# Kernel tuning notes

Hardware: AMD Instinct MI355X
Metric: run time of the kernel (lower is better)

The kernel has to match this reference:

```python
import jax, jax.numpy as jnp
import numpy as np

NUM_TNETS = 8388608
NUM_PINS = 20971520
NUM_NODES = 1048576

def setup_inputs() -> dict:
    key = jax.random.key(0)
    k1, k2, k3 = jax.random.split(key, 3)
    beta = jax.random.uniform(k1, (1,), dtype=jnp.float32)
    tnet_weights = jax.random.uniform(k2, (NUM_TNETS,), dtype=jnp.float32)
    flat_tnet2pin = jax.random.randint(k3, (2 * NUM_TNETS,), 0, NUM_PINS, dtype=jnp.int64)
    pin2node_map = jax.random.randint(jax.random.fold_in(key, 7), (NUM_PINS,), 0, NUM_NODES, dtype=jnp.int64)
    return {
        "beta": beta,
        "tnet_weights": tnet_weights,
        "flat_tnet2pin": flat_tnet2pin,
        "pin2node_map": pin2node_map,
    }

def reference(beta, tnet_weights, flat_tnet2pin, pin2node_map):
    # flat_tnet2pin layout: [src_0, dst_0, src_1, dst_1, ...] (2 pins per timing arc)
    # gather node id for every arc pin: [2*num_tnets]
    node_idx = pin2node_map[flat_tnet2pin]
    # each arc's weight is added at both its source and sink node
    w = jnp.repeat(tnet_weights, 2)  # [w0, w0, w1, w1, ...] matches flat layout
    out = jnp.zeros(NUM_NODES, dtype=jnp.float32).at[node_idx].add(w)
    return out * beta
```

## Files before the change

kernel.cpp:

```cpp
#include <hip/hip_runtime.h>
#include <stdint.h>


#define TILE 4096
#define THREADS 512
#define IPT  8
#define NB1  40
#define SHIFT1 19
#define CAP1R 55296
#define TPB1R 14
#define NB2  64
#define SHIFT2 14
#define CAP2R 34816
#define ACC_NODES 16384
#define PARTS 8
#define CLINE_INTS 16
#define TICK1_OFF 65536
#define TICK2_OFF 66048
#define CTRL_BYTES 66560
#define NT2R (5 * 8 * TPB1R)

typedef unsigned long long item_t;
typedef int   int4_ev   __attribute__((ext_vector_type(4)));
typedef float float4_ev __attribute__((ext_vector_type(4)));
typedef unsigned long long ull2_ev __attribute__((ext_vector_type(2)));

#define BAR() do { __builtin_amdgcn_sched_barrier(0); \
    asm volatile("s_waitcnt lgkmcnt(0)" ::: "memory"); \
    __builtin_amdgcn_s_barrier(); \
    __builtin_amdgcn_sched_barrier(0); } while (0)

__device__ __forceinline__ item_t pack_item(uint32_t key, float w) {
    return (item_t)key | ((item_t)__float_as_uint(w) << 32);
}

__device__ __forceinline__ void ms_passA(item_t (&e)[IPT], int vcnt, int shift,
                                         int* hist, uint32_t (&rankp)[IPT / 2]) {
#pragma unroll
    for (int k = 0; k < IPT; ++k) {
        int b = (int)((uint32_t)e[k] >> shift);
        uint32_t rr = (k < vcnt) ? (uint32_t)atomicAdd(&hist[b], 1) : 0u;
        if ((k & 1) == 0) rankp[k >> 1] = rr;
        else              rankp[k >> 1] |= (rr << 16);
    }
}

__device__ __forceinline__ void ms_scan(int t, int* hist, unsigned long long* combo,
                                        int* wsum, int* gcur, int gcur_stride) {
    int val = (t < 256) ? hist[t] : 0;
    int inc = val;
#pragma unroll
    for (int d = 1; d < 64; d <<= 1) {
        int n = __shfl_up(inc, d, 64);
        if ((t & 63) >= d) inc += n;
    }
    if (t < 256 && (t & 63) == 63) wsum[t >> 6] = inc;
    BAR();
    if (t < 256) {
        hist[t] = 0;
        int w = t >> 6, prefix = 0;
        if (w > 0) prefix += wsum[0];
        if (w > 1) prefix += wsum[1];
        if (w > 2) prefix += wsum[2];
        int bx = prefix + inc - val;
        int gb = (val > 0) ? atomicAdd(&gcur[t * gcur_stride], val) : 0;
        combo[t] = ((unsigned long long)(uint32_t)gb << 32) | (uint32_t)bx;
    }
}

__device__ __forceinline__ void ms_passD(item_t (&e)[IPT], int vcnt, int shift,
                                         uint32_t (&rankp)[IPT / 2],
                                         unsigned long long* combo, item_t* stage) {
#pragma unroll
    for (int k = 0; k < IPT; ++k) {
        if (k < vcnt) {
            int b = (int)((uint32_t)e[k] >> shift);
            int rr = (int)((rankp[k >> 1] >> ((k & 1) * 16)) & 0xffffu);
            stage[(int)((uint32_t)combo[b]) + rr] = e[k];
        }
    }
}

__device__ __forceinline__ void ms_passE(int t, item_t* stage, int tile_cnt, int shift,
                                         unsigned long long* combo,
                                         item_t* gout, size_t bin_stride, size_t cap) {
    for (int j = t; j < tile_cnt; j += THREADS) {
        item_t ev = stage[j];
        int b = (int)((uint32_t)(ev & 0xffffffffull) >> shift);
        unsigned long long c = combo[b];
        long long dst = (long long)(int)(c >> 32) + (j - (int)(uint32_t)c);
        if (dst >= 0 && dst < (long long)cap)
            __builtin_nontemporal_store(ev, &gout[(size_t)b * bin_stride + (size_t)dst]);
    }
}

__global__ __launch_bounds__(THREADS, 8) void k1_partition_pins(
    const int* __restrict__ flat_pins, const float* __restrict__ weights,
    int* __restrict__ ctrl1, int* __restrict__ tick1,
    item_t* __restrict__ items1, int total)
{
    __shared__ int hist[256];
    __shared__ unsigned long long combo[256];
    __shared__ int wsum[4];
    __shared__ item_t stage[TILE];
    __shared__ int sh_tk;

    const int t = threadIdx.x;
    const int r = blockIdx.x & 7;
    const int gridTiles = (total + TILE - 1) / TILE;
    const int ntr = (gridTiles > r) ? ((gridTiles - r + 7) >> 3) : 0;
    int* mytick = tick1 + r * CLINE_INTS;
    int* mycur  = ctrl1 + r * CLINE_INTS;
    item_t* mout = items1 + (size_t)r * CAP1R;

    if (t == 0) sh_tk = atomicAdd(mytick, 1);
    if (t < 256) hist[t] = 0;
    __syncthreads();
    if (sh_tk >= ntr) return;

    item_t e[IPT];
    int vcnt, tcnt;
    {
        int tb = (r + (sh_tk << 3)) * TILE;
        int base = tb + t * IPT;
        tcnt = min(TILE, total - tb);
        if (base + IPT <= total) {
            vcnt = IPT;
            int4_ev p0 = __builtin_nontemporal_load((const int4_ev*)(flat_pins + base));
            int4_ev p1 = __builtin_nontemporal_load((const int4_ev*)(flat_pins + base) + 1);
            float4_ev w = __builtin_nontemporal_load((const float4_ev*)(weights + (base >> 1)));
#pragma unroll
            for (int k = 0; k < IPT; ++k)
                e[k] = pack_item((uint32_t)((k < 4) ? p0[k & 3] : p1[k & 3]), w[(k >> 1) & 3]);
        } else {
            int rem = total - base;
            vcnt = rem < 0 ? 0 : (rem > IPT ? IPT : rem);
#pragma unroll
            for (int k = 0; k < IPT; ++k) {
                int i = base + k;
                e[k] = (i < total) ? pack_item((uint32_t)flat_pins[i], weights[i >> 1]) : 0ull;
            }
        }
    }
    __syncthreads();

    for (;;) {
        int tkf = 0x7fffffff;
        if (t == 0) tkf = atomicAdd(mytick, 1);
        uint32_t rankp[IPT / 2];
        ms_passA(e, vcnt, SHIFT1, hist, rankp);
        BAR();
        ms_scan(t, hist, combo, wsum, mycur, 8 * CLINE_INTS);
        if (t == 0) sh_tk = tkf;
        BAR();
        ms_passD(e, vcnt, SHIFT1, rankp, combo, stage);
        BAR();
        const int tkn = sh_tk;
        const bool valid = (tkn < ntr);
        int4_ev px0, px1; float4_ev wx;
        bool fastN = false; int baseN = 0, tbN = 0;
        if (valid) {
            tbN = (r + (tkn << 3)) * TILE;
            baseN = tbN + t * IPT;
            fastN = (baseN + IPT <= total);
            if (fastN) {
                px0 = __builtin_nontemporal_load((const int4_ev*)(flat_pins + baseN));
                px1 = __builtin_nontemporal_load((const int4_ev*)(flat_pins + baseN) + 1);
                wx  = __builtin_nontemporal_load((const float4_ev*)(weights + (baseN >> 1)));
            }
        }
        ms_passE(t, stage, tcnt, SHIFT1, combo, mout, (size_t)8 * CAP1R, (size_t)CAP1R);
        BAR();
        if (!valid) break;
        tcnt = min(TILE, total - tbN);
        if (fastN) {
            vcnt = IPT;
#pragma unroll
            for (int k = 0; k < IPT; ++k)
                e[k] = pack_item((uint32_t)((k < 4) ? px0[k & 3] : px1[k & 3]), wx[(k >> 1) & 3]);
        } else {
            int rem = total - baseN;
            vcnt = rem < 0 ? 0 : (rem > IPT ? IPT : rem);
#pragma unroll
            for (int k = 0; k < IPT; ++k) {
                int i = baseN + k;
                e[k] = (i < total) ? pack_item((uint32_t)flat_pins[i], weights[i >> 1]) : 0ull;
            }
        }
    }
}

__global__ __launch_bounds__(THREADS, 8) void k2_gather_partition(
    const item_t* __restrict__ items1, const int* __restrict__ ctrl1,
    const int* __restrict__ pin2node, int* __restrict__ ctrl2,
    int* __restrict__ tick2, item_t* __restrict__ items2)
{
    __shared__ int hist[256];
    __shared__ unsigned long long combo[256];
    __shared__ int wsum[4];
    __shared__ item_t stage[TILE];
    __shared__ int sh_tk;
    __shared__ int sh_cnt[NB1];

    const int t = threadIdx.x;
    const int r2 = blockIdx.x & 7;
    int* mytick = tick2 + r2 * CLINE_INTS;
    int* mycur  = ctrl2 + r2 * CLINE_INTS;
    item_t* mout = items2 + (size_t)r2 * CAP2R;

    if (t == 0) sh_tk = atomicAdd(mytick, 1);
    if (t < 256) hist[t] = 0;
    if (t < NB1) {
        int bin = r2 + 8 * (t >> 3);
        sh_cnt[t] = min(ctrl1[(bin * 8 + (t & 7)) * CLINE_INTS], (int)CAP1R);
    }
    __syncthreads();
    if (sh_tk >= NT2R) return;

#define GMERGE(slot, ev_) { item_t ev = (ev_); \
        int nd = pin2node[(uint32_t)ev]; \
        e[slot] = (ev & 0xffffffff00000000ull) | (uint32_t)nd; }

    item_t e[IPT];
    int vcnt, tcnt;
    {
        int tk = sh_tk;
        int g = tk / (8 * TPB1R), rem = tk % (8 * TPB1R);
        int r_w = rem / TPB1R, tile = rem % TPB1R;
        int bin = r2 + 8 * g;
        int cnt = sh_cnt[(g << 3) | r_w];
        int tb = tile * TILE;
        tcnt = max(0, min(TILE, cnt - tb));
        const item_t* src = items1 + ((size_t)bin * 8 + (size_t)r_w) * CAP1R;
        int base = tb + t * IPT;
        if (base + IPT <= cnt) {
            vcnt = IPT;
            ull2_ev x0 = __builtin_nontemporal_load((const ull2_ev*)(src + base));
            ull2_ev x1 = __builtin_nontemporal_load((const ull2_ev*)(src + base) + 1);
            ull2_ev x2 = __builtin_nontemporal_load((const ull2_ev*)(src + base) + 2);
            ull2_ev x3 = __builtin_nontemporal_load((const ull2_ev*)(src + base) + 3);
            GMERGE(0, x0[0]) GMERGE(1, x0[1]) GMERGE(2, x1[0]) GMERGE(3, x1[1])
            GMERGE(4, x2[0]) GMERGE(5, x2[1]) GMERGE(6, x3[0]) GMERGE(7, x3[1])
        } else {
            int rem2 = cnt - base;
            vcnt = rem2 < 0 ? 0 : (rem2 > IPT ? IPT : rem2);
#pragma unroll
            for (int k = 0; k < IPT; ++k) {
                int i = base + k;
                if (i >= 0 && i < cnt) { GMERGE(k, src[i]) } else e[k] = 0ull;
            }
        }
    }
    __syncthreads();

    for (;;) {
        int tkf = 0x7fffffff;
        if (t == 0) tkf = atomicAdd(mytick, 1);
        uint32_t rankp[IPT / 2];
        ms_passA(e, vcnt, SHIFT2, hist, rankp);
        BAR();
        ms_scan(t, hist, combo, wsum, mycur, 8 * CLINE_INTS);
        if (t == 0) sh_tk = tkf;
        BAR();
        ms_passD(e, vcnt, SHIFT2, rankp, combo, stage);
        BAR();
        const int tkn = sh_tk;
        const bool valid = (tkn < NT2R);
        ull2_ev nx0, nx1, nx2, nx3;
        bool fastN = false;
        const item_t* srcN = items1;
        int baseN = 0, cntN = 0, tbN = 0;
        if (valid) {
            int g = tkn / (8 * TPB1R), rem = tkn % (8 * TPB1R);
            int r_w = rem / TPB1R, tile = rem % TPB1R;
            int bin = r2 + 8 * g;
            cntN = sh_cnt[(g << 3) | r_w];
            tbN = tile * TILE;
            srcN = items1 + ((size_t)bin * 8 + (size_t)r_w) * CAP1R;
            baseN = tbN + t * IPT;
            fastN = (baseN + IPT <= cntN);
            if (fastN) {
                nx0 = __builtin_nontemporal_load((const ull2_ev*)(srcN + baseN));
                nx1 = __builtin_nontemporal_load((const ull2_ev*)(srcN + baseN) + 1);
                nx2 = __builtin_nontemporal_load((const ull2_ev*)(srcN + baseN) + 2);
                nx3 = __builtin_nontemporal_load((const ull2_ev*)(srcN + baseN) + 3);
            }
        }
        ms_passE(t, stage, tcnt, SHIFT2, combo, mout, (size_t)8 * CAP2R, (size_t)CAP2R);
        BAR();
        if (!valid) break;
        tcnt = max(0, min(TILE, cntN - tbN));
        if (fastN) {
            vcnt = IPT;
            GMERGE(0, nx0[0]) GMERGE(1, nx0[1]) GMERGE(2, nx1[0]) GMERGE(3, nx1[1])
            GMERGE(4, nx2[0]) GMERGE(5, nx2[1]) GMERGE(6, nx3[0]) GMERGE(7, nx3[1])
        } else {
            int rem2 = cntN - baseN;
            vcnt = rem2 < 0 ? 0 : (rem2 > IPT ? IPT : rem2);
#pragma unroll
            for (int k = 0; k < IPT; ++k) {
                int i = baseN + k;
                if (i >= 0 && i < cntN) { GMERGE(k, srcN[i]) } else e[k] = 0ull;
            }
        }
    }
#undef GMERGE
}

__global__ __launch_bounds__(1024, 8) void k3_accumulate_part(
    const item_t* __restrict__ items2, const int* __restrict__ ctrl2,
    float* __restrict__ partials)
{
    __shared__ float acc[ACC_NODES];
    const int b = blockIdx.x >> 3;
    const int p = blockIdx.x & (PARTS - 1);
    const int t = threadIdx.x;
    for (int i = t; i < ACC_NODES; i += 1024) acc[i] = 0.f;
    __syncthreads();

    const int cnt = min(ctrl2[(b * 8 + p) * CLINE_INTS], (int)CAP2R);
    const item_t* src = items2 + ((size_t)b * 8 + (size_t)p) * CAP2R;
    const ull2_ev* src2 = (const ull2_ev*)src;
    const int npair = cnt >> 1;
    const int quarter = npair >> 2;

#define K3_LOAD(A0, A1, A2, A3, g) { \
    A0 = __builtin_nontemporal_load(src2 + (g)); \
    A1 = __builtin_nontemporal_load(src2 + quarter + (g)); \
    A2 = __builtin_nontemporal_load(src2 + 2 * quarter + (g)); \
    A3 = __builtin_nontemporal_load(src2 + 3 * quarter + (g)); }
#define K3_ACC1(ev) atomicAdd(&acc[(uint32_t)(ev) & (ACC_NODES - 1)], \
                              __uint_as_float((uint32_t)((ev) >> 32)))
#define K3_PROC(A0, A1, A2, A3) { \
    K3_ACC1(A0[0]); K3_ACC1(A0[1]); K3_ACC1(A1[0]); K3_ACC1(A1[1]); \
    K3_ACC1(A2[0]); K3_ACC1(A2[1]); K3_ACC1(A3[0]); K3_ACC1(A3[1]); }

    ull2_ev a0, a1, a2, a3, b0, b1, b2, b3;
    int g = t;
    bool vA = g < quarter;
    if (vA) K3_LOAD(a0, a1, a2, a3, g)
    int gB = g + 1024;
    while (vA) {
        bool vB = gB < quarter;
        if (vB) K3_LOAD(b0, b1, b2, b3, gB)
        K3_PROC(a0, a1, a2, a3)
        g = gB + 1024;
        vA = g < quarter;
        if (vA) K3_LOAD(a0, a1, a2, a3, g)
        if (vB) K3_PROC(b0, b1, b2, b3)
        gB = g + 1024;
    }
    for (int i = (quarter << 3) + t; i < cnt; i += 1024) {
        item_t ev = src[i];
        K3_ACC1(ev);
    }
#undef K3_LOAD
#undef K3_ACC1
#undef K3_PROC
    __syncthreads();
    float* __restrict__ dst = partials + (size_t)blockIdx.x * ACC_NODES;
    for (int i = t; i < ACC_NODES; i += 1024) dst[i] = acc[i];
}

__global__ __launch_bounds__(256) void k4_reduce(
    const float* __restrict__ partials, const float* __restrict__ beta,
    float* __restrict__ out, int num_nodes)
{
    const float bt = beta[0];
    const int n = (blockIdx.x * 256 + threadIdx.x) << 2;
    if (n + 3 < num_nodes) {
        const int b   = n >> SHIFT2;
        const int off = n & (ACC_NODES - 1);
        const float* base = partials + ((size_t)b * PARTS) * ACC_NODES + off;
        float4_ev s = {0.f, 0.f, 0.f, 0.f};
#pragma unroll
        for (int p = 0; p < PARTS; ++p)
            s += *(const float4_ev*)(base + (size_t)p * ACC_NODES);
        *(float4_ev*)(out + n) = s * bt;
    } else {
        for (int k = 0; k < 4; ++k) {
            int nn = n + k;
            if (nn < num_nodes) {
                const int b   = nn >> SHIFT2;
                const int off = nn & (ACC_NODES - 1);
                float s = 0.f;
#pragma unroll
                for (int p = 0; p < PARTS; ++p)
                    s += partials[((size_t)b * PARTS + p) * ACC_NODES + off];
                out[nn] = s * bt;
            }
        }
    }
}

__global__ __launch_bounds__(256) void scatter_device(
    const float* __restrict__ beta, const float* __restrict__ tnet_weights,
    const long long* __restrict__ pin_pairs, const int* __restrict__ pin2node_map,
    float* __restrict__ out, int num_tnets)
{
    int t = blockIdx.x * blockDim.x + threadIdx.x;
    if (t >= num_tnets) return;
    long long pp = pin_pairs[t];
    float w = tnet_weights[t] * beta[0];
    atomicAdd(&out[pin2node_map[(int)(pp & 0xffffffffLL)]], w);
    atomicAdd(&out[pin2node_map[(int)(pp >> 32)]], w);
}

extern "C" void kernel_launch(void* const* d_in, const int* in_sizes, int n_in,
                              void* d_out, int out_size, void* d_ws, size_t ws_size,
                              hipStream_t stream) {
    const float* beta         = (const float*)d_in[0];
    const float* weights      = (const float*)d_in[1];
    const int*   flat_pins    = (const int*)d_in[2];
    const int*   pin2node     = (const int*)d_in[3];
    float* out = (float*)d_out;

    const int num_tnets = in_sizes[1];
    const int total     = in_sizes[2];
    const int num_nodes = out_size;

    const size_t items1Bytes = (size_t)NB1 * 8 * CAP1R * sizeof(item_t);
    const size_t items2Bytes = (size_t)NB2 * 8 * CAP2R * sizeof(item_t);
    const size_t partBytes   = (size_t)NB2 * PARTS * ACC_NODES * sizeof(float);

    int* ctrl1 = (int*)d_ws;
    int* ctrl2 = (int*)((char*)d_ws + 32768);
    int* tick1 = (int*)((char*)d_ws + TICK1_OFF);
    int* tick2 = (int*)((char*)d_ws + TICK2_OFF);

    if (ws_size >= CTRL_BYTES + items1Bytes + items2Bytes + partBytes) {
        item_t* items1 = (item_t*)((char*)d_ws + CTRL_BYTES);
        item_t* items2 = (item_t*)((char*)d_ws + CTRL_BYTES + items1Bytes);
        float*  partials = (float*)((char*)d_ws + CTRL_BYTES + items1Bytes + items2Bytes);
        (void)hipMemsetAsync(d_ws, 0, CTRL_BYTES, stream);
        k1_partition_pins<<<1024, THREADS, 0, stream>>>(
            flat_pins, weights, ctrl1, tick1, items1, total);
        k2_gather_partition<<<1024, THREADS, 0, stream>>>(
            items1, ctrl1, pin2node, ctrl2, tick2, items2);
        k3_accumulate_part<<<NB2 * PARTS, 1024, 0, stream>>>(
            items2, ctrl2, partials);
        const int i4slots = (num_nodes + 3) / 4;
        k4_reduce<<<(i4slots + 255) / 256, 256, 0, stream>>>(
            partials, beta, out, num_nodes);
    } else {
        (void)hipMemsetAsync(d_out, 0, (size_t)out_size * sizeof(float), stream);
        scatter_device<<<(num_tnets + 255) / 256, 256, 0, stream>>>(
            beta, weights, (const long long*)flat_pins, pin2node, out, num_tnets);
    }
}
```

Before: 464.6 us.

## Replace atomic ticket work-stealing with static two-tile-per-block assignment in partition kernels

The persistent 1024-block grids in the first two partition kernels, which grab tiles through per-residue atomic tickets, are replaced by grids sized so each block handles exactly two statically assigned tiles. The next tile's loads are still issued before the scatter of the current tile. This removes the per-iteration atomic ticket traffic and the tick counters in the workspace, which also shrinks the memset. In exchange it launches many more blocks, pays per-block setup and histogram init again for each pair of tiles, and loses dynamic load balancing.

After: 466.5 us. No clear change (+0.4%).

```diff
diff --git a/kernel.cpp b/kernel.cpp
--- a/kernel.cpp
+++ b/kernel.cpp
@@ -15,10 +15,8 @@
 #define ACC_NODES 16384
 #define PARTS 8
 #define CLINE_INTS 16
-#define TICK1_OFF 65536
-#define TICK2_OFF 66048
-#define CTRL_BYTES 66560
-#define NT2R (5 * 8 * TPB1R)
+#define CTRL_BYTES 65536
+#define SPR2 (5 * 8 * TPB1R)
 
 typedef unsigned long long item_t;
 typedef int   int4_ev   __attribute__((ext_vector_type(4)));
@@ -94,216 +92,153 @@
     }
 }
 
+__device__ __forceinline__ void k1_load(
+    const int* __restrict__ flat_pins, const float* __restrict__ weights,
+    int total, int tb, int t, item_t (&e)[IPT], int& vcnt, int& tcnt)
+{
+    const int base = tb + t * IPT;
+    int tc = total - tb; tc = tc < 0 ? 0 : (tc > TILE ? TILE : tc);
+    tcnt = tc;
+    if (base + IPT <= total) {
+        vcnt = IPT;
+        int4_ev p0 = __builtin_nontemporal_load((const int4_ev*)(flat_pins + base));
+        int4_ev p1 = __builtin_nontemporal_load((const int4_ev*)(flat_pins + base) + 1);
+        float4_ev w = __builtin_nontemporal_load((const float4_ev*)(weights + (base >> 1)));
+#pragma unroll
+        for (int k = 0; k < IPT; ++k)
+            e[k] = pack_item((uint32_t)((k < 4) ? p0[k & 3] : p1[k & 3]), w[(k >> 1) & 3]);
+    } else {
+        int rem = total - base;
+        vcnt = rem < 0 ? 0 : (rem > IPT ? IPT : rem);
+#pragma unroll
+        for (int k = 0; k < IPT; ++k) {
+            int i = base + k;
+            e[k] = (i < total) ? pack_item((uint32_t)flat_pins[i], weights[i >> 1]) : 0ull;
+        }
+    }
+}
+
 __global__ __launch_bounds__(THREADS, 8) void k1_partition_pins(
     const int* __restrict__ flat_pins, const float* __restrict__ weights,
-    int* __restrict__ ctrl1, int* __restrict__ tick1,
-    item_t* __restrict__ items1, int total)
+    int* __restrict__ ctrl1, item_t* __restrict__ items1, int total)
 {
     __shared__ int hist[256];
     __shared__ unsigned long long combo[256];
     __shared__ int wsum[4];
     __shared__ item_t stage[TILE];
-    __shared__ int sh_tk;
 
     const int t = threadIdx.x;
     const int r = blockIdx.x & 7;
-    const int gridTiles = (total + TILE - 1) / TILE;
-    const int ntr = (gridTiles > r) ? ((gridTiles - r + 7) >> 3) : 0;
-    int* mytick = tick1 + r * CLINE_INTS;
-    int* mycur  = ctrl1 + r * CLINE_INTS;
+    const int sp = blockIdx.x >> 3;
+    int* mycur = ctrl1 + r * CLINE_INTS;
     item_t* mout = items1 + (size_t)r * CAP1R;
 
-    if (t == 0) sh_tk = atomicAdd(mytick, 1);
     if (t < 256) hist[t] = 0;
-    __syncthreads();
-    if (sh_tk >= ntr) return;
 
     item_t e[IPT];
     int vcnt, tcnt;
-    {
-        int tb = (r + (sh_tk << 3)) * TILE;
-        int base = tb + t * IPT;
-        tcnt = min(TILE, total - tb);
-        if (base + IPT <= total) {
-            vcnt = IPT;
-            int4_ev p0 = __builtin_nontemporal_load((const int4_ev*)(flat_pins + base));
-            int4_ev p1 = __builtin_nontemporal_load((const int4_ev*)(flat_pins + base) + 1);
-            float4_ev w = __builtin_nontemporal_load((const float4_ev*)(weights + (base >> 1)));
-#pragma unroll
-            for (int k = 0; k < IPT; ++k)
-                e[k] = pack_item((uint32_t)((k < 4) ? p0[k & 3] : p1[k & 3]), w[(k >> 1) & 3]);
-        } else {
-            int rem = total - base;
-            vcnt = rem < 0 ? 0 : (rem > IPT ? IPT : rem);
-#pragma unroll
-            for (int k = 0; k < IPT; ++k) {
-                int i = base + k;
-                e[k] = (i < total) ? pack_item((uint32_t)flat_pins[i], weights[i >> 1]) : 0ull;
-            }
-        }
-    }
+    const int j0 = r + 8 * (2 * sp);
+    k1_load(flat_pins, weights, total, j0 * TILE, t, e, vcnt, tcnt);
     __syncthreads();
 
-    for (;;) {
-        int tkf = 0x7fffffff;
-        if (t == 0) tkf = atomicAdd(mytick, 1);
+#pragma unroll 1
+    for (int it = 0; it < 2; ++it) {
         uint32_t rankp[IPT / 2];
         ms_passA(e, vcnt, SHIFT1, hist, rankp);
         BAR();
         ms_scan(t, hist, combo, wsum, mycur, 8 * CLINE_INTS);
-        if (t == 0) sh_tk = tkf;
         BAR();
         ms_passD(e, vcnt, SHIFT1, rankp, combo, stage);
         BAR();
-        const int tkn = sh_tk;
-        const bool valid = (tkn < ntr);
-        int4_ev px0, px1; float4_ev wx;
-        bool fastN = false; int baseN = 0, tbN = 0;
-        if (valid) {
-            tbN = (r + (tkn << 3)) * TILE;
-            baseN = tbN + t * IPT;
-            fastN = (baseN + IPT <= total);
-            if (fastN) {
-                px0 = __builtin_nontemporal_load((const int4_ev*)(flat_pins + baseN));
-                px1 = __builtin_nontemporal_load((const int4_ev*)(flat_pins + baseN) + 1);
-                wx  = __builtin_nontemporal_load((const float4_ev*)(weights + (baseN >> 1)));
-            }
-        }
-        ms_passE(t, stage, tcnt, SHIFT1, combo, mout, (size_t)8 * CAP1R, (size_t)CAP1R);
-        BAR();
-        if (!valid) break;
-        tcnt = min(TILE, total - tbN);
-        if (fastN) {
-            vcnt = IPT;
-#pragma unroll
-            for (int k = 0; k < IPT; ++k)
-                e[k] = pack_item((uint32_t)((k < 4) ? px0[k & 3] : px1[k & 3]), wx[(k >> 1) & 3]);
-        } else {
-            int rem = total - baseN;
-            vcnt = rem < 0 ? 0 : (rem > IPT ? IPT : rem);
-#pragma unroll
-            for (int k = 0; k < IPT; ++k) {
-                int i = baseN + k;
-                e[k] = (i < total) ? pack_item((uint32_t)flat_pins[i], weights[i >> 1]) : 0ull;
-            }
-        }
+        const int tcnt_cur = tcnt;
+        if (it == 0) {
+            k1_load(flat_pins, weights, total, (j0 + 8) * TILE, t, e, vcnt, tcnt);
+        }
+        ms_passE(t, stage, tcnt_cur, SHIFT1, combo, mout,
+                 (size_t)8 * CAP1R, (size_t)CAP1R);
+        BAR();
     }
 }
 
 __global__ __launch_bounds__(THREADS, 8) void k2_gather_partition(
     const item_t* __restrict__ items1, const int* __restrict__ ctrl1,
-    const int* __restrict__ pin2node, int* __restrict__ ctrl2,
-    int* __restrict__ tick2, item_t* __restrict__ items2)
+    const int* __restrict__ pin2node,
+    int* __restrict__ ctrl2, item_t* __restrict__ items2)
 {
     __shared__ int hist[256];
     __shared__ unsigned long long combo[256];
     __shared__ int wsum[4];
     __shared__ item_t stage[TILE];
-    __shared__ int sh_tk;
     __shared__ int sh_cnt[NB1];
 
     const int t = threadIdx.x;
     const int r2 = blockIdx.x & 7;
-    int* mytick = tick2 + r2 * CLINE_INTS;
-    int* mycur  = ctrl2 + r2 * CLINE_INTS;
+    const int sp = blockIdx.x >> 3;
+    int* mycur = ctrl2 + r2 * CLINE_INTS;
     item_t* mout = items2 + (size_t)r2 * CAP2R;
 
-    if (t == 0) sh_tk = atomicAdd(mytick, 1);
     if (t < 256) hist[t] = 0;
     if (t < NB1) {
         int bin = r2 + 8 * (t >> 3);
         sh_cnt[t] = min(ctrl1[(bin * 8 + (t & 7)) * CLINE_INTS], (int)CAP1R);
     }
     __syncthreads();
-    if (sh_tk >= NT2R) return;
 
 #define GMERGE(slot, ev_) { item_t ev = (ev_); \
         int nd = pin2node[(uint32_t)ev]; \
         e[slot] = (ev & 0xffffffff00000000ull) | (uint32_t)nd; }
 
+#define K2_LOAD(sidx) { \
+        int s_ = (sidx); \
+        int g_ = s_ / (8 * TPB1R), rem_ = s_ % (8 * TPB1R); \
+        int rw_ = rem_ / TPB1R, tile_ = rem_ % TPB1R; \
+        int bin_ = r2 + 8 * g_; \
+        int cnt_ = sh_cnt[(g_ << 3) | rw_]; \
+        int tb_ = tile_ * TILE; \
+        int tc_ = cnt_ - tb_; tc_ = tc_ < 0 ? 0 : (tc_ > TILE ? TILE : tc_); \
+        tcnt = tc_; \
+        const item_t* src_ = items1 + ((size_t)bin_ * 8 + (size_t)rw_) * CAP1R; \
+        int base_ = tb_ + t * IPT; \
+        if (base_ + IPT <= cnt_) { \
+            vcnt = IPT; \
+            ull2_ev x0 = __builtin_nontemporal_load((const ull2_ev*)(src_ + base_)); \
+            ull2_ev x1 = __builtin_nontemporal_load((const ull2_ev*)(src_ + base_) + 1); \
+            ull2_ev x2 = __builtin_nontemporal_load((const ull2_ev*)(src_ + base_) + 2); \
+            ull2_ev x3 = __builtin_nontemporal_load((const ull2_ev*)(src_ + base_) + 3); \
+            GMERGE(0, x0[0]) GMERGE(1, x0[1]) GMERGE(2, x1[0]) GMERGE(3, x1[1]) \
+            GMERGE(4, x2[0]) GMERGE(5, x2[1]) GMERGE(6, x3[0]) GMERGE(7, x3[1]) \
+        } else { \
+            int rem2_ = cnt_ - base_; \
+            vcnt = rem2_ < 0 ? 0 : (rem2_ > IPT ? IPT : rem2_); \
+            _Pragma("unroll") \
+            for (int k = 0; k < IPT; ++k) { \
+                int i_ = base_ + k; \
+                if (i_ < cnt_) { GMERGE(k, src_[i_]) } else e[k] = 0ull; \
+            } \
+        } }
+
     item_t e[IPT];
     int vcnt, tcnt;
-    {
-        int tk = sh_tk;
-        int g = tk / (8 * TPB1R), rem = tk % (8 * TPB1R);
-        int r_w = rem / TPB1R, tile = rem % TPB1R;
-        int bin = r2 + 8 * g;
-        int cnt = sh_cnt[(g << 3) | r_w];
-        int tb = tile * TILE;
-        tcnt = max(0, min(TILE, cnt - tb));
-        const item_t* src = items1 + ((size_t)bin * 8 + (size_t)r_w) * CAP1R;
-        int base = tb + t * IPT;
-        if (base + IPT <= cnt) {
-            vcnt = IPT;
-            ull2_ev x0 = __builtin_nontemporal_load((const ull2_ev*)(src + base));
-            ull2_ev x1 = __builtin_nontemporal_load((const ull2_ev*)(src + base) + 1);
-            ull2_ev x2 = __builtin_nontemporal_load((const ull2_ev*)(src + base) + 2);
-            ull2_ev x3 = __builtin_nontemporal_load((const ull2_ev*)(src + base) + 3);
-            GMERGE(0, x0[0]) GMERGE(1, x0[1]) GMERGE(2, x1[0]) GMERGE(3, x1[1])
-            GMERGE(4, x2[0]) GMERGE(5, x2[1]) GMERGE(6, x3[0]) GMERGE(7, x3[1])
-        } else {
-            int rem2 = cnt - base;
-            vcnt = rem2 < 0 ? 0 : (rem2 > IPT ? IPT : rem2);
-#pragma unroll
-            for (int k = 0; k < IPT; ++k) {
-                int i = base + k;
-                if (i >= 0 && i < cnt) { GMERGE(k, src[i]) } else e[k] = 0ull;
-            }
-        }
-    }
-    __syncthreads();
-
-    for (;;) {
-        int tkf = 0x7fffffff;
-        if (t == 0) tkf = atomicAdd(mytick, 1);
+    K2_LOAD(2 * sp);
+
+#pragma unroll 1
+    for (int it = 0; it < 2; ++it) {
         uint32_t rankp[IPT / 2];
         ms_passA(e, vcnt, SHIFT2, hist, rankp);
         BAR();
         ms_scan(t, hist, combo, wsum, mycur, 8 * CLINE_INTS);
-        if (t == 0) sh_tk = tkf;
         BAR();
         ms_passD(e, vcnt, SHIFT2, rankp, combo, stage);
         BAR();
-        const int tkn = sh_tk;
-        const bool valid = (tkn < NT2R);
-        ull2_ev nx0, nx1, nx2, nx3;
-        bool fastN = false;
-        const item_t* srcN = items1;
-        int baseN = 0, cntN = 0, tbN = 0;
-        if (valid) {
-            int g = tkn / (8 * TPB1R), rem = tkn % (8 * TPB1R);
-            int r_w = rem / TPB1R, tile = rem % TPB1R;
-            int bin = r2 + 8 * g;
-            cntN = sh_cnt[(g << 3) | r_w];
-            tbN = tile * TILE;
-            srcN = items1 + ((size_t)bin * 8 + (size_t)r_w) * CAP1R;
-            baseN = tbN + t * IPT;
-            fastN = (baseN + IPT <= cntN);
-            if (fastN) {
-                nx0 = __builtin_nontemporal_load((const ull2_ev*)(srcN + baseN));
-                nx1 = __builtin_nontemporal_load((const ull2_ev*)(srcN + baseN) + 1);
-                nx2 = __builtin_nontemporal_load((const ull2_ev*)(srcN + baseN) + 2);
-                nx3 = __builtin_nontemporal_load((const ull2_ev*)(srcN + baseN) + 3);
-            }
-        }
-        ms_passE(t, stage, tcnt, SHIFT2, combo, mout, (size_t)8 * CAP2R, (size_t)CAP2R);
-        BAR();
-        if (!valid) break;
-        tcnt = max(0, min(TILE, cntN - tbN));
-        if (fastN) {
-            vcnt = IPT;
-            GMERGE(0, nx0[0]) GMERGE(1, nx0[1]) GMERGE(2, nx1[0]) GMERGE(3, nx1[1])
-            GMERGE(4, nx2[0]) GMERGE(5, nx2[1]) GMERGE(6, nx3[0]) GMERGE(7, nx3[1])
-        } else {
-            int rem2 = cntN - baseN;
-            vcnt = rem2 < 0 ? 0 : (rem2 > IPT ? IPT : rem2);
-#pragma unroll
-            for (int k = 0; k < IPT; ++k) {
-                int i = baseN + k;
-                if (i >= 0 && i < cntN) { GMERGE(k, srcN[i]) } else e[k] = 0ull;
-            }
-        }
-    }
+        const int tcnt_cur = tcnt;
+        if (it == 0) {
+            K2_LOAD(2 * sp + 1);
+        }
+        ms_passE(t, stage, tcnt_cur, SHIFT2, combo, mout,
+                 (size_t)8 * CAP2R, (size_t)CAP2R);
+        BAR();
+    }
+#undef K2_LOAD
 #undef GMERGE
 }
 
@@ -425,18 +360,20 @@
 
     int* ctrl1 = (int*)d_ws;
     int* ctrl2 = (int*)((char*)d_ws + 32768);
-    int* tick1 = (int*)((char*)d_ws + TICK1_OFF);
-    int* tick2 = (int*)((char*)d_ws + TICK2_OFF);
 
     if (ws_size >= CTRL_BYTES + items1Bytes + items2Bytes + partBytes) {
         item_t* items1 = (item_t*)((char*)d_ws + CTRL_BYTES);
         item_t* items2 = (item_t*)((char*)d_ws + CTRL_BYTES + items1Bytes);
         float*  partials = (float*)((char*)d_ws + CTRL_BYTES + items1Bytes + items2Bytes);
         (void)hipMemsetAsync(d_ws, 0, CTRL_BYTES, stream);
-        k1_partition_pins<<<1024, THREADS, 0, stream>>>(
-            flat_pins, weights, ctrl1, tick1, items1, total);
-        k2_gather_partition<<<1024, THREADS, 0, stream>>>(
-            items1, ctrl1, pin2node, ctrl2, tick2, items2);
+
+        const int gridTiles = (total + TILE - 1) / TILE;
+        const int tilesPerRes = (gridTiles + 7) / 8;
+        const int k1Blocks = 8 * ((tilesPerRes + 1) / 2);
+        k1_partition_pins<<<k1Blocks, THREADS, 0, stream>>>(
+            flat_pins, weights, ctrl1, items1, total);
+        k2_gather_partition<<<8 * (SPR2 / 2), THREADS, 0, stream>>>(
+            items1, ctrl1, pin2node, ctrl2, items2);
         k3_accumulate_part<<<NB2 * PARTS, 1024, 0, stream>>>(
             items2, ctrl2, partials);
         const int i4slots = (num_nodes + 3) / 4;
```
